# Kernel optimization log

Hardware: AMD Instinct MI355X
Metric: run time of the kernel (lower is better)

## Reference

```python
import jax, jax.numpy as jnp
import numpy as np
from jax import lax

H = W = 28

def _bilinear(img, yy, xx, zero_pad):
    # img [C,H,W]; yy/xx [H,W] fractional source coords
    y0 = jnp.floor(yy); x0 = jnp.floor(xx)
    wy = yy - y0; wx = xx - x0
    y0i = y0.astype(jnp.int32); x0i = x0.astype(jnp.int32)
    def gather(yi, xi):
        v = img[:, jnp.clip(yi, 0, H - 1), jnp.clip(xi, 0, W - 1)]
        if zero_pad:
            valid = ((yi >= 0) & (yi < H) & (xi >= 0) & (xi < W)).astype(img.dtype)
            v = v * valid[None]
        return v
    return (gather(y0i, x0i) * (1 - wy) * (1 - wx)
            + gather(y0i, x0i + 1) * (1 - wy) * wx
            + gather(y0i + 1, x0i) * wy * (1 - wx)
            + gather(y0i + 1, x0i + 1) * wy * wx)

def _crop_resize(img, crop, top, left):
    # bilinear resize of img[:, top:top+crop, left:left+crop] back to 28x28
    # (same math as F.interpolate align_corners=False with edge clamping)
    j = jnp.arange(H, dtype=jnp.float32) + 0.5
    src = jnp.clip(j * crop / H - 0.5, 0.0, crop - 1.0)
    yy, xx = jnp.meshgrid(src + top, src + left, indexing='ij')
    return _bilinear(img, yy, xx, zero_pad=False)

def _rotate(img, rad):
    # F.affine_grid/grid_sample, align_corners=False, zero padding
    c = (2.0 * jnp.arange(H, dtype=jnp.float32) + 1.0) / H - 1.0
    Yn, Xn = jnp.meshgrid(c, c, indexing='ij')
    cs, sn = jnp.cos(rad), jnp.sin(rad)
    xs = cs * Xn - sn * Yn
    ys = sn * Xn + cs * Yn
    ix = ((xs + 1.0) * W - 1.0) / 2.0
    iy = ((ys + 1.0) * H - 1.0) / 2.0
    return _bilinear(img, iy, ix, zero_pad=True)

def augment(x, key):
    # fully batched version of the per-sample python-loop augmentation
    B = x.shape[0]
    ks = jax.random.split(key, 11)
    u = lambda k: jax.random.uniform(k, (B,))
    crop = jnp.floor(28.0 * (0.7 + 0.3 * u(ks[0])))          # int(28*(0.7+0.3*r))
    top = jnp.floor((28.0 - crop) * u(ks[1]))
    left = jnp.floor((28.0 - crop) * u(ks[2]))
    x = jax.vmap(_crop_resize)(x, crop, top, left)
    flip = (u(ks[3]) < 0.5)[:, None, None, None]
    x = jnp.where(flip, x[..., ::-1], x)
    rot = (u(ks[4]) < 0.8)[:, None, None, None]
    rad = (20.0 * u(ks[5]) - 10.0) * jnp.pi / 180.0
    x = jnp.where(rot, jax.vmap(_rotate)(x, rad), x)
    cj = (u(ks[6]) < 0.8)[:, None, None, None]
    b = (0.2 * u(ks[7]) - 0.1)[:, None, None, None]
    c = (0.8 + 0.4 * u(ks[8]))[:, None, None, None]
    xj = jnp.clip((jnp.clip(x + b, 0.0, 1.0) - 0.5) * c + 0.5, 0.0, 1.0)
    x = jnp.where(cj, xj, x)
    na = (u(ks[9]) < 0.5)[:, None, None, None]
    noise = 0.05 * jax.random.normal(ks[10], x.shape, dtype=x.dtype)
    x = jnp.where(na, jnp.clip(x + noise, 0.0, 1.0), x)
    return (x - 0.5) / 0.5

def _conv(x, Wc, bc):
    y = lax.conv_general_dilated(x, Wc, (1, 1), 'SAME',
                                 dimension_numbers=('NCHW', 'OIHW', 'NCHW'))
    return y + bc[None, :, None, None]

def _maxpool2(x):
    return lax.reduce_window(x, -jnp.inf, lax.max, (1, 1, 2, 2), (1, 1, 2, 2), 'VALID')

def encoder(x, W1, b1, W2, b2, Wf, bf):
    h = _maxpool2(jax.nn.relu(_conv(x, W1, b1)))   # [B,32,14,14]
    h = _maxpool2(jax.nn.relu(_conv(h, W2, b2)))   # [B,64,7,7]
    h = h.reshape(h.shape[0], -1)                  # [B,3136]
    return h @ Wf.T + bf                           # [B,512]

def projector(h, Wp1, bp1, Wp2, bp2):
    return jax.nn.relu(h @ Wp1.T + bp1) @ Wp2.T + bp2

def setup_inputs() -> dict:
    key = jax.random.key(0)
    ks = jax.random.split(key, 12)
    B, FD, PD = 4096, 512, 128
    x = jax.random.uniform(ks[0], (B, 1, 28, 28), dtype=jnp.float32)
    s = lambda k, shp, fan: (jax.random.normal(k, shp, dtype=jnp.float32) * (1.0 / np.sqrt(fan)))
    return {
        'x': x,
        'W1': s(ks[1], (32, 1, 3, 3), 9), 'b1': jnp.zeros((32,), jnp.float32),
        'W2': s(ks[2], (64, 32, 3, 3), 32 * 9), 'b2': jnp.zeros((64,), jnp.float32),
        'Wf': s(ks[3], (FD, 64 * 7 * 7), 64 * 7 * 7), 'bf': jnp.zeros((FD,), jnp.float32),
        'Wp1': s(ks[4], (FD, FD), FD), 'bp1': jnp.zeros((FD,), jnp.float32),
        'Wp2': s(ks[5], (PD, FD), FD), 'bp2': jnp.zeros((PD,), jnp.float32),
    }

def reference(x, W1, b1, W2, b2, Wf, bf, Wp1, bp1, Wp2, bp2):
    akey = jax.random.key(42)
    k1, k2 = jax.random.split(akey)
    x1 = augment(x, k1)
    x2 = augment(x, k2)
    h1 = encoder(x1, W1, b1, W2, b2, Wf, bf)
    h2 = encoder(x2, W1, b1, W2, b2, Wf, bf)
    z1 = projector(h1, Wp1, bp1, Wp2, bp2)
    z2 = projector(h2, Wp1, bp1, Wp2, bp2)
    return (z1, z2)
```

## Files before the change

### kernel.cpp

```cpp
#include <hip/hip_runtime.h>
#include <stdint.h>
#include <math.h>

typedef __attribute__((ext_vector_type(8))) short bf16x8;
typedef __attribute__((ext_vector_type(4))) float f32x4;

__device__ __forceinline__ ushort f2bf(float f) {
    uint32_t u = __float_as_uint(f);
    u += 0x7fffu + ((u >> 16) & 1u);
    return (ushort)(u >> 16);
}

__device__ __forceinline__ uint32_t rotl32(uint32_t v, int r) {
    return (v << r) | (v >> (32 - r));
}

__device__ __forceinline__ void threefry(uint32_t k0, uint32_t k1,
                                         uint32_t c0, uint32_t c1,
                                         uint32_t& o0, uint32_t& o1) {
    uint32_t ks2 = k0 ^ k1 ^ 0x1BD11BDAu;
    uint32_t x0 = c0 + k0, x1 = c1 + k1;
    x0 += x1; x1 = rotl32(x1, 13); x1 ^= x0;
    x0 += x1; x1 = rotl32(x1, 15); x1 ^= x0;
    x0 += x1; x1 = rotl32(x1, 26); x1 ^= x0;
    x0 += x1; x1 = rotl32(x1,  6); x1 ^= x0;
    x0 += k1;  x1 += ks2 + 1u;
    x0 += x1; x1 = rotl32(x1, 17); x1 ^= x0;
    x0 += x1; x1 = rotl32(x1, 29); x1 ^= x0;
    x0 += x1; x1 = rotl32(x1, 16); x1 ^= x0;
    x0 += x1; x1 = rotl32(x1, 24); x1 ^= x0;
    x0 += ks2; x1 += k0 + 2u;
    x0 += x1; x1 = rotl32(x1, 13); x1 ^= x0;
    x0 += x1; x1 = rotl32(x1, 15); x1 ^= x0;
    x0 += x1; x1 = rotl32(x1, 26); x1 ^= x0;
    x0 += x1; x1 = rotl32(x1,  6); x1 ^= x0;
    x0 += k0;  x1 += k1 + 3u;
    x0 += x1; x1 = rotl32(x1, 17); x1 ^= x0;
    x0 += x1; x1 = rotl32(x1, 29); x1 ^= x0;
    x0 += x1; x1 = rotl32(x1, 16); x1 ^= x0;
    x0 += x1; x1 = rotl32(x1, 24); x1 ^= x0;
    x0 += k1;  x1 += ks2 + 4u;
    x0 += x1; x1 = rotl32(x1, 13); x1 ^= x0;
    x0 += x1; x1 = rotl32(x1, 15); x1 ^= x0;
    x0 += x1; x1 = rotl32(x1, 26); x1 ^= x0;
    x0 += x1; x1 = rotl32(x1,  6); x1 ^= x0;
    x0 += ks2; x1 += k0 + 5u;
    o0 = x0; o1 = x1;
}

__device__ __forceinline__ uint32_t rbits32(uint32_t k0, uint32_t k1, uint32_t idx) {
    uint32_t o0, o1;
    threefry(k0, k1, 0u, idx, o0, o1);
    return o0 ^ o1;
}

__device__ __forceinline__ float u01_from_bits(uint32_t bits) {
    return __uint_as_float((bits >> 9) | 0x3f800000u) - 1.0f;
}

__device__ float erfinv_xla(float x) {
    #pragma clang fp contract(off)
    float w = -log1pf(-x * x);
    float p;
    if (w < 5.0f) {
        w = w - 2.5f;
        p = 2.81022636e-08f;
        p = 3.43273939e-07f + p * w;
        p = -3.5233877e-06f + p * w;
        p = -4.39150654e-06f + p * w;
        p = 0.00021858087f + p * w;
        p = -0.00125372503f + p * w;
        p = -0.00417768164f + p * w;
        p = 0.246640727f + p * w;
        p = 1.50140941f + p * w;
    } else {
        w = sqrtf(w) - 3.0f;
        p = -0.000200214257f;
        p = 0.000100950558f + p * w;
        p = 0.00134934322f + p * w;
        p = -0.00367342844f + p * w;
        p = 0.00573950773f + p * w;
        p = -0.0076224613f + p * w;
        p = 0.00943887047f + p * w;
        p = 1.00167406f + p * w;
        p = 2.83297682f + p * w;
    }
    return p * x;
}

#define P_OFF      0
#define NK_OFF     98304
#define W2GT_OFF   98320
#define WFB_OFF    107792
#define WP1B_OFF   910608
#define WP2B_OFF   1041680
#define AUG_OFF    1074448
#define PL2_OFF    4285712
#define H_OFF      10708240

__global__ void param_kernel(float* __restrict__ P, uint32_t* __restrict__ NK) {
    #pragma clang fp contract(off)
    int gid = blockIdx.x * blockDim.x + threadIdx.x;
    if (gid >= 8192) return;
    int v = gid >> 12;
    int i = gid & 4095;

    uint32_t kv0, kv1;
    threefry(0u, 42u, 0u, (uint32_t)v, kv0, kv1);

    uint32_t sk0[11], sk1[11];
    #pragma unroll
    for (int j = 0; j < 11; ++j) threefry(kv0, kv1, 0u, (uint32_t)j, sk0[j], sk1[j]);

    float u[10];
    #pragma unroll
    for (int j = 0; j < 10; ++j) u[j] = u01_from_bits(rbits32(sk0[j], sk1[j], (uint32_t)i));

    float crop = floorf(28.0f * (0.7f + 0.3f * u[0]));
    float top  = floorf((28.0f - crop) * u[1]);
    float left = floorf((28.0f - crop) * u[2]);
    float flip = (u[3] < 0.5f) ? 1.0f : 0.0f;
    float rot  = (u[4] < 0.8f) ? 1.0f : 0.0f;
    float rad  = ((20.0f * u[5] - 10.0f) * 3.14159274101257324f) / 180.0f;
    float cj   = (u[6] < 0.8f) ? 1.0f : 0.0f;
    float bb   = 0.2f * u[7] - 0.1f;
    float cc   = 0.8f + 0.4f * u[8];
    float na   = (u[9] < 0.5f) ? 1.0f : 0.0f;

    float* p = P + gid * 12;
    p[0] = crop; p[1] = top; p[2] = left; p[3] = flip; p[4] = rot;
    p[5] = rad;  p[6] = cj;  p[7] = bb;   p[8] = cc;   p[9] = na;
    p[10] = cosf(rad); p[11] = sinf(rad);

    if (i == 0) { NK[v * 2] = sk0[10]; NK[v * 2 + 1] = sk1[10]; }
}

__global__ void wprep_w2(const float* __restrict__ W2, ushort* __restrict__ W2gT) {
    int idx = blockIdx.x * 256 + threadIdx.x;
    if (idx >= 64 * 296) return;
    int oc = idx / 296, k = idx % 296;
    float v = 0.0f;
    if (k < 288) {
        int s = k >> 5, ic = k & 31;
        int ky = s / 3, kx = s % 3;
        v = W2[((oc * 32 + ic) * 3 + ky) * 3 + kx];
    }
    W2gT[idx] = f2bf(v);
}

__global__ void wprep_wf(const float* __restrict__ Wf, ushort* __restrict__ WfB) {
    int idx = blockIdx.x * 256 + threadIdx.x;
    if (idx >= 512 * 3136) return;
    int n = idx / 3136, kp = idx % 3136;
    int pos = kp >> 6, oc = kp & 63;
    WfB[idx] = f2bf(Wf[n * 3136 + oc * 49 + pos]);
}

__global__ void wprep_cast(const float* __restrict__ src, ushort* __restrict__ dst, int n) {
    int idx = blockIdx.x * 256 + threadIdx.x;
    if (idx < n) dst[idx] = f2bf(src[idx]);
}

__global__ __launch_bounds__(256) void augment_kernel(const float* __restrict__ x,
                                                      const float* __restrict__ P,
                                                      const uint32_t* __restrict__ NK,
                                                      float* __restrict__ AUG, int v) {
    #pragma clang fp contract(off)
    int i = blockIdx.x;
    int r = v * 4096 + i;
    int t = threadIdx.x;
    __shared__ float img[784];
    __shared__ float s1[784];
    __shared__ float srctab[28];

    const float* p = P + r * 12;
    float crop = p[0], top = p[1], left = p[2];
    int flip = (p[3] != 0.0f);
    int rot  = (p[4] != 0.0f);
    int cj = (p[6] != 0.0f);
    float bb = p[7], cc = p[8];
    int na = (p[9] != 0.0f);
    float cs = p[10], sn = p[11];
    uint32_t nk0 = NK[v * 2], nk1 = NK[v * 2 + 1];

    for (int q = t; q < 784; q += 256) img[q] = x[i * 784 + q];
    if (t < 28) {
        float j = (float)t + 0.5f;
        float s = j * crop / 28.0f - 0.5f;
        srctab[t] = fminf(fmaxf(s, 0.0f), crop - 1.0f);
    }
    __syncthreads();

    for (int q = t; q < 784; q += 256) {
        int py = q / 28, px = q - (q / 28) * 28;
        int sxcol = flip ? (27 - px) : px;
        float yy = srctab[py] + top;
        float xx = srctab[sxcol] + left;
        float y0f = floorf(yy), x0f = floorf(xx);
        float wy = yy - y0f, wx = xx - x0f;
        int y0 = (int)y0f, x0 = (int)x0f;

        int yc0 = min(max(y0, 0), 27),     xc0 = min(max(x0, 0), 27);
        int yc1 = min(max(y0 + 1, 0), 27), xc1 = min(max(x0 + 1, 0), 27);
        float g00 = img[yc0 * 28 + xc0];
        float g01 = img[yc0 * 28 + xc1];
        float g10 = img[yc1 * 28 + xc0];
        float g11 = img[yc1 * 28 + xc1];
        float val = g00 * (1.0f - wy) * (1.0f - wx) + g01 * (1.0f - wy) * wx
                  + g10 * wy * (1.0f - wx) + g11 * wy * wx;
        s1[q] = val;
    }
    __syncthreads();

    for (int q = t; q < 784; q += 256) {
        int py = q / 28, px = q - (q / 28) * 28;
        float val;
        if (rot) {
            float Yn = (2.0f * (float)py + 1.0f) / 28.0f - 1.0f;
            float Xn = (2.0f * (float)px + 1.0f) / 28.0f - 1.0f;
            float xs = cs * Xn - sn * Yn;
            float ys = sn * Xn + cs * Yn;
            float ix = ((xs + 1.0f) * 28.0f - 1.0f) / 2.0f;
            float iy = ((ys + 1.0f) * 28.0f - 1.0f) / 2.0f;
            float y0f = floorf(iy), x0f = floorf(ix);
            float wy = iy - y0f, wx = ix - x0f;
            int y0 = (int)y0f, x0 = (int)x0f;
            float g[2][2];
            #pragma unroll
            for (int dy = 0; dy < 2; ++dy) {
                #pragma unroll
                for (int dx = 0; dx < 2; ++dx) {
                    int yi = y0 + dy, xi = x0 + dx;
                    int yc = min(max(yi, 0), 27), xc = min(max(xi, 0), 27);
                    float vv = s1[yc * 28 + xc];
                    float valid = (yi >= 0 && yi < 28 && xi >= 0 && xi < 28) ? 1.0f : 0.0f;
                    g[dy][dx] = vv * valid;
                }
            }
            val = g[0][0] * (1.0f - wy) * (1.0f - wx) + g[0][1] * (1.0f - wy) * wx
                + g[1][0] * wy * (1.0f - wx) + g[1][1] * wy * wx;
        } else {
            val = s1[q];
        }

        if (cj) {
            float vc = fminf(fmaxf(val + bb, 0.0f), 1.0f);
            val = fminf(fmaxf((vc - 0.5f) * cc + 0.5f, 0.0f), 1.0f);
        }

        if (na) {
            int idx = i * 784 + q;
            uint32_t bits = rbits32(nk0, nk1, (uint32_t)idx);
            float f = u01_from_bits(bits);
            const float lo = -0.99999994f;
            float uu = f * 2.0f + lo;
            uu = fmaxf(lo, uu);
            float n = 1.4142135623730951f * erfinv_xla(uu);
            val = fminf(fmaxf(val + 0.05f * n, 0.0f), 1.0f);
        }

        AUG[i * 784 + q] = (val - 0.5f) / 0.5f;
    }
}

__global__ __launch_bounds__(256) void conv12_kernel(
        const float* __restrict__ AUG,
        const float* __restrict__ W1, const float* __restrict__ b1,
        const ushort* __restrict__ W2gT, const float* __restrict__ b2,
        ushort* __restrict__ PL2) {
    int i = blockIdx.x, t = threadIdx.x;
    __shared__ __align__(16) ushort buf[12576];
    __shared__ __align__(16) ushort w1sT[32 * 32];
    ushort* A1   = buf;
    ushort* pl1p = buf;

    {
        int q0 = t * 4;
        #pragma unroll
        for (int j = 0; j < 4; ++j) {
            int q = q0 + j;
            int oc = q >> 5, k = q & 31;
            w1sT[q] = (k < 9) ? f2bf(W1[oc * 9 + k]) : (ushort)0;
        }
    }

    const float* Ai = AUG + (size_t)i * 784;
    if (t < 196) {
        int py = t / 14, px = t - (t / 14) * 14;
        int ybase = 2 * py - 1, xbase = 2 * px - 1;
        uint32_t u[4][4];
        #pragma unroll
        for (int ry = 0; ry < 4; ++ry) {
            int yy = ybase + ry;
            bool yok = (unsigned)yy < 28u;
            const float* rowp = Ai + yy * 28;
            #pragma unroll
            for (int rx = 0; rx < 4; ++rx) {
                int xx = xbase + rx;
                float vv = (yok && (unsigned)xx < 28u) ? rowp[xx] : 0.0f;
                u[ry][rx] = (uint32_t)f2bf(vv);
            }
        }
        #pragma unroll
        for (int w = 0; w < 4; ++w) {
            int dy = w >> 1, dx = w & 1;
            uint4 W0, W1v;
            W0.x = u[dy][dx]     | (u[dy][dx + 1] << 16);
            W0.y = u[dy][dx + 2] | (u[dy + 1][dx] << 16);
            W0.z = u[dy + 1][dx + 1] | (u[dy + 1][dx + 2] << 16);
            W0.w = u[dy + 2][dx]     | (u[dy + 2][dx + 1] << 16);
            W1v.x = u[dy + 2][dx + 2];
            W1v.y = 0; W1v.z = 0; W1v.w = 0;
            ((uint4*)A1)[(t * 4 + w) * 2]     = W0;
            ((uint4*)A1)[(t * 4 + w) * 2 + 1] = W1v;
        }
    }
    __syncthreads();

    int l = t & 63, wv = t >> 6;
    int lr = l & 15, lg = l >> 4;

    float m0r[13], m1r[13];
    {
        bf16x8 bA = *(const bf16x8*)(w1sT + lr * 32 + lg * 8);
        bf16x8 bB = *(const bf16x8*)(w1sT + (16 + lr) * 32 + lg * 8);
        #pragma unroll
        for (int it = 0; it < 13; ++it) {
            int tt = wv + it * 4;
            if (tt < 49) {
                bf16x8 af = *(const bf16x8*)(A1 + (tt * 16 + lr) * 16 + lg * 8);
                f32x4 a0 = {0.0f, 0.0f, 0.0f, 0.0f};
                f32x4 a1acc = {0.0f, 0.0f, 0.0f, 0.0f};
                a0    = __builtin_amdgcn_mfma_f32_16x16x32_bf16(af, bA, a0, 0, 0, 0);
                a1acc = __builtin_amdgcn_mfma_f32_16x16x32_bf16(af, bB, a1acc, 0, 0, 0);
                m0r[it] = fmaxf(fmaxf(a0[0], a0[1]), fmaxf(a0[2], a0[3]));
                m1r[it] = fmaxf(fmaxf(a1acc[0], a1acc[1]), fmaxf(a1acc[2], a1acc[3]));
            }
        }
    }
    __syncthreads();

    for (int q = t; q < 1440; q += 256) ((uint4*)pl1p)[q] = uint4{0, 0, 0, 0};
    __syncthreads();

    {
        float bia0 = b1[lr], bia1 = b1[16 + lr];
        #pragma unroll
        for (int it = 0; it < 13; ++it) {
            int tt = wv + it * 4;
            if (tt < 49) {
                int pidx = tt * 4 + lg;
                int py = pidx / 14, px = pidx - py * 14;
                int base = ((py + 1) * 18 + (px + 1)) * 40;
                pl1p[base + lr]      = f2bf(fmaxf(m0r[it] + bia0, 0.0f));
                pl1p[base + 16 + lr] = f2bf(fmaxf(m1r[it] + bia1, 0.0f));
            }
        }
    }
    __syncthreads();

    {
        bf16x8 bfr[9];
        #pragma unroll
        for (int s = 0; s < 9; ++s)
            bfr[s] = *(const bf16x8*)(W2gT + (wv * 16 + lr) * 296 + s * 32 + lg * 8);
        float bias2 = b2[wv * 16 + lr];

        #pragma unroll
        for (int pyp = 0; pyp < 7; ++pyp) {
            int py0 = pyp * 2;
            bf16x8 f[4][3];
            #pragma unroll
            for (int j = 0; j < 4; ++j)
                #pragma unroll
                for (int kx = 0; kx < 3; ++kx)
                    f[j][kx] = *(const bf16x8*)(pl1p + ((py0 + j) * 18 + (lr + kx)) * 40 + lg * 8);
            f32x4 acc0 = {bias2, bias2, bias2, bias2};
            f32x4 acc1 = acc0;
            #pragma unroll
            for (int ky = 0; ky < 3; ++ky)
                #pragma unroll
                for (int kx = 0; kx < 3; ++kx) {
                    acc0 = __builtin_amdgcn_mfma_f32_16x16x32_bf16(f[ky][kx],     bfr[ky * 3 + kx], acc0, 0, 0, 0);
                    acc1 = __builtin_amdgcn_mfma_f32_16x16x32_bf16(f[ky + 1][kx], bfr[ky * 3 + kx], acc1, 0, 0, 0);
                }
            float v0 = fmaxf(fmaxf(fmaxf(acc0[0], acc0[1]), fmaxf(acc1[0], acc1[1])), 0.0f);
            float v1 = fmaxf(fmaxf(fmaxf(acc0[2], acc0[3]), fmaxf(acc1[2], acc1[3])), 0.0f);
            int px0 = lg * 2, px1 = px0 + 1;
            size_t base = (size_t)i * 3136 + (size_t)(pyp * 7) * 64 + wv * 16 + lr;
            PL2[base + (size_t)px0 * 64] = f2bf(v0);
            if (px1 < 7) PL2[base + (size_t)px1 * 64] = f2bf(v1);
        }
    }
}

template<bool RELU, bool OUT_BF16>
__global__ __launch_bounds__(256) void gemm_bt_kernel(
        const ushort* __restrict__ A, const ushort* __restrict__ BT,
        const float* __restrict__ bias, void* __restrict__ Cout,
        int M, int N, int K) {
    __shared__ __align__(16) ushort lds[2][2][4096];
    int t = threadIdx.x;
    int w = t >> 6, l = t & 63;
    int lr = l & 15, lc = l >> 4;
    int wm = w >> 1, wn = w & 1;
    int bm = blockIdx.x, bn = blockIdx.y;
    int NKt = K >> 6;

    const ushort* Ab = A + (size_t)bm * 64 * K;
    const ushort* Bb = BT + (size_t)bn * 64 * K;

    int r0 = t >> 3, s0 = t & 7;
    int c1i = t + 256;
    int r1 = c1i >> 3, s1 = c1i & 7;
    int d0 = r0 * 8 + (s0 ^ (r0 & 7));
    int d1 = r1 * 8 + (s1 ^ (r1 & 7));

    f32x4 acc[2][2] = {};

    uint4 tA0, tA1, tB0, tB1;
    #define GLOAD(kt) do { \
        tA0 = *(const uint4*)(Ab + (size_t)r0 * K + (kt) * 64 + s0 * 8); \
        tA1 = *(const uint4*)(Ab + (size_t)r1 * K + (kt) * 64 + s1 * 8); \
        tB0 = *(const uint4*)(Bb + (size_t)r0 * K + (kt) * 64 + s0 * 8); \
        tB1 = *(const uint4*)(Bb + (size_t)r1 * K + (kt) * 64 + s1 * 8); } while (0)
    #define LWRITE(bufi) do { \
        ((uint4*)lds[bufi][0])[d0] = tA0; ((uint4*)lds[bufi][0])[d1] = tA1; \
        ((uint4*)lds[bufi][1])[d0] = tB0; ((uint4*)lds[bufi][1])[d1] = tB1; } while (0)

    GLOAD(0); LWRITE(0);
    int buf = 0;
    for (int kt = 0; kt < NKt; ++kt) {
        __syncthreads();
        if (kt + 1 < NKt) GLOAD(kt + 1);
        const ushort* Al = lds[buf][0];
        const ushort* Bl = lds[buf][1];
        #pragma unroll
        for (int ks = 0; ks < 2; ++ks) {
            bf16x8 af[2], bg[2];
            #pragma unroll
            for (int mt = 0; mt < 2; ++mt) {
                int row = wm * 32 + mt * 16 + lr;
                int unit = row * 8 + ((ks * 4 + lc) ^ (row & 7));
                af[mt] = *(const bf16x8*)(Al + unit * 8);
            }
            #pragma unroll
            for (int nt = 0; nt < 2; ++nt) {
                int row = wn * 32 + nt * 16 + lr;
                int unit = row * 8 + ((ks * 4 + lc) ^ (row & 7));
                bg[nt] = *(const bf16x8*)(Bl + unit * 8);
            }
            #pragma unroll
            for (int mt = 0; mt < 2; ++mt)
                #pragma unroll
                for (int nt = 0; nt < 2; ++nt)
                    acc[mt][nt] = __builtin_amdgcn_mfma_f32_16x16x32_bf16(af[mt], bg[nt], acc[mt][nt], 0, 0, 0);
        }
        if (kt + 1 < NKt) LWRITE(buf ^ 1);
        buf ^= 1;
    }

    #pragma unroll
    for (int nt = 0; nt < 2; ++nt) {
        int gcol = bn * 64 + wn * 32 + nt * 16 + lr;
        float bv = bias[gcol];
        #pragma unroll
        for (int mt = 0; mt < 2; ++mt) {
            #pragma unroll
            for (int rg = 0; rg < 4; ++rg) {
                int grow = bm * 64 + wm * 32 + mt * 16 + lc * 4 + rg;
                float vv = acc[mt][nt][rg] + bv;
                if (RELU) vv = fmaxf(vv, 0.0f);
                if (OUT_BF16) ((ushort*)Cout)[(size_t)grow * N + gcol] = f2bf(vv);
                else          ((float*)Cout)[(size_t)grow * N + gcol] = vv;
            }
        }
    }
    #undef GLOAD
    #undef LWRITE
}

extern "C" void kernel_launch(void* const* d_in, const int* in_sizes, int n_in,
                              void* d_out, int out_size, void* d_ws, size_t ws_size,
                              hipStream_t stream) {
    const float* x   = (const float*)d_in[0];
    const float* W1  = (const float*)d_in[1];
    const float* b1  = (const float*)d_in[2];
    const float* W2  = (const float*)d_in[3];
    const float* b2  = (const float*)d_in[4];
    const float* Wf  = (const float*)d_in[5];
    const float* bf  = (const float*)d_in[6];
    const float* Wp1 = (const float*)d_in[7];
    const float* bp1 = (const float*)d_in[8];
    const float* Wp2 = (const float*)d_in[9];
    const float* bp2 = (const float*)d_in[10];

    float* ws     = (float*)d_ws;
    float* P      = ws + P_OFF;
    uint32_t* NK  = (uint32_t*)(ws + NK_OFF);
    ushort* W2gT  = (ushort*)(ws + W2GT_OFF);
    ushort* WfB   = (ushort*)(ws + WFB_OFF);
    ushort* Wp1B  = (ushort*)(ws + WP1B_OFF);
    ushort* Wp2B  = (ushort*)(ws + WP2B_OFF);
    float* AUG    = ws + AUG_OFF;
    ushort* PL2   = (ushort*)(ws + PL2_OFF);
    ushort* Hb    = (ushort*)(ws + H_OFF);
    ushort* P1    = (ushort*)(ws + AUG_OFF);
    float* out    = (float*)d_out;

    param_kernel<<<32, 256, 0, stream>>>(P, NK);
    wprep_w2<<<74, 256, 0, stream>>>(W2, W2gT);
    wprep_wf<<<6272, 256, 0, stream>>>(Wf, WfB);
    wprep_cast<<<1024, 256, 0, stream>>>(Wp1, Wp1B, 512 * 512);
    wprep_cast<<<256, 256, 0, stream>>>(Wp2, Wp2B, 128 * 512);

    for (int v = 0; v < 2; ++v) {
        augment_kernel<<<4096, 256, 0, stream>>>(x, P, NK, AUG, v);
        conv12_kernel<<<4096, 256, 0, stream>>>(AUG, W1, b1, W2gT, b2, PL2);
        gemm_bt_kernel<false, true><<<dim3(64, 8), 256, 0, stream>>>(
            PL2, WfB, bf, Hb, 4096, 512, 3136);
        gemm_bt_kernel<true, true><<<dim3(64, 8), 256, 0, stream>>>(
            Hb, Wp1B, bp1, P1, 4096, 512, 512);
        gemm_bt_kernel<false, false><<<dim3(64, 2), 256, 0, stream>>>(
            P1, Wp2B, bp2, out + (size_t)v * 4096 * 128, 4096, 128, 512);
    }
}
```

Before: 261.4 us.

## Add 128x64-tile bf16 GEMM kernel for encoder FC and projector layer

Adds a new GEMM kernel with 128-row M tiles, where each wave computes a 64x32 output block (4x2 MFMA tiles). It uses swizzled LDS and register-staged double buffering, and is applied to the encoder FC and the first projector GEMM. The larger tile raises arithmetic intensity and halves the number of B-tile reloads across M. In exchange, the grid shrinks to 256 blocks, which may underfill the GPU's CUs, and register pressure goes up.

```diff
diff --git a/kernel.cpp b/kernel.cpp
--- a/kernel.cpp
+++ b/kernel.cpp
@@ -395,6 +395,97 @@
 }
 
 template<bool RELU, bool OUT_BF16>
+__global__ __launch_bounds__(256) void gemm_bt128_kernel(
+        const ushort* __restrict__ A, const ushort* __restrict__ BT,
+        const float* __restrict__ bias, void* __restrict__ Cout,
+        int M, int N, int K) {
+    __shared__ __align__(16) ushort lds[2][12288];
+    int t = threadIdx.x;
+    int w = t >> 6, l = t & 63;
+    int lr = l & 15, lc = l >> 4;
+    int wm = w >> 1, wn = w & 1;
+    int bm = blockIdx.x, bn = blockIdx.y;
+    int NKt = K >> 6;
+
+    const ushort* Ab = A + (size_t)bm * 128 * K;
+    const ushort* Bb = BT + (size_t)bn * 64 * K;
+
+    int rA[4], sA[4], dA[4];
+    #pragma unroll
+    for (int j = 0; j < 4; ++j) {
+        int idx = t + 256 * j;
+        rA[j] = idx >> 3; sA[j] = idx & 7;
+        dA[j] = rA[j] * 8 + (sA[j] ^ (rA[j] & 7));
+    }
+
+    f32x4 acc[4][2] = {};
+
+    uint4 tA[4], tB[2];
+    #define GLOAD(kt) do { \
+        tA[0] = *(const uint4*)(Ab + (size_t)rA[0] * K + (kt) * 64 + sA[0] * 8); \
+        tA[1] = *(const uint4*)(Ab + (size_t)rA[1] * K + (kt) * 64 + sA[1] * 8); \
+        tA[2] = *(const uint4*)(Ab + (size_t)rA[2] * K + (kt) * 64 + sA[2] * 8); \
+        tA[3] = *(const uint4*)(Ab + (size_t)rA[3] * K + (kt) * 64 + sA[3] * 8); \
+        tB[0] = *(const uint4*)(Bb + (size_t)rA[0] * K + (kt) * 64 + sA[0] * 8); \
+        tB[1] = *(const uint4*)(Bb + (size_t)rA[1] * K + (kt) * 64 + sA[1] * 8); } while (0)
+    #define LWRITE(bufi) do { \
+        ((uint4*)lds[bufi])[dA[0]] = tA[0]; ((uint4*)lds[bufi])[dA[1]] = tA[1]; \
+        ((uint4*)lds[bufi])[dA[2]] = tA[2]; ((uint4*)lds[bufi])[dA[3]] = tA[3]; \
+        ((uint4*)lds[bufi])[1024 + dA[0]] = tB[0]; ((uint4*)lds[bufi])[1024 + dA[1]] = tB[1]; } while (0)
+
+    GLOAD(0); LWRITE(0);
+    int buf = 0;
+    for (int kt = 0; kt < NKt; ++kt) {
+        __syncthreads();
+        if (kt + 1 < NKt) GLOAD(kt + 1);
+        const ushort* Al = lds[buf];
+        const ushort* Bl = lds[buf] + 8192;
+        #pragma unroll
+        for (int ks = 0; ks < 2; ++ks) {
+            bf16x8 af[4], bg[2];
+            #pragma unroll
+            for (int mt = 0; mt < 4; ++mt) {
+                int row = wm * 64 + mt * 16 + lr;
+                int unit = row * 8 + ((ks * 4 + lc) ^ (row & 7));
+                af[mt] = *(const bf16x8*)(Al + unit * 8);
+            }
+            #pragma unroll
+            for (int nt = 0; nt < 2; ++nt) {
+                int row = wn * 32 + nt * 16 + lr;
+                int unit = row * 8 + ((ks * 4 + lc) ^ (row & 7));
+                bg[nt] = *(const bf16x8*)(Bl + unit * 8);
+            }
+            #pragma unroll
+            for (int mt = 0; mt < 4; ++mt)
+                #pragma unroll
+                for (int nt = 0; nt < 2; ++nt)
+                    acc[mt][nt] = __builtin_amdgcn_mfma_f32_16x16x32_bf16(af[mt], bg[nt], acc[mt][nt], 0, 0, 0);
+        }
+        if (kt + 1 < NKt) LWRITE(buf ^ 1);
+        buf ^= 1;
+    }
+
+    #pragma unroll
+    for (int nt = 0; nt < 2; ++nt) {
+        int gcol = bn * 64 + wn * 32 + nt * 16 + lr;
+        float bv = bias[gcol];
+        #pragma unroll
+        for (int mt = 0; mt < 4; ++mt) {
+            #pragma unroll
+            for (int rg = 0; rg < 4; ++rg) {
+                int grow = bm * 128 + wm * 64 + mt * 16 + lc * 4 + rg;
+                float vv = acc[mt][nt][rg] + bv;
+                if (RELU) vv = fmaxf(vv, 0.0f);
+                if (OUT_BF16) ((ushort*)Cout)[(size_t)grow * N + gcol] = f2bf(vv);
+                else          ((float*)Cout)[(size_t)grow * N + gcol] = vv;
+            }
+        }
+    }
+    #undef GLOAD
+    #undef LWRITE
+}
+
+template<bool RELU, bool OUT_BF16>
 __global__ __launch_bounds__(256) void gemm_bt_kernel(
         const ushort* __restrict__ A, const ushort* __restrict__ BT,
         const float* __restrict__ bias, void* __restrict__ Cout,
@@ -517,9 +608,9 @@
     for (int v = 0; v < 2; ++v) {
         augment_kernel<<<4096, 256, 0, stream>>>(x, P, NK, AUG, v);
         conv12_kernel<<<4096, 256, 0, stream>>>(AUG, W1, b1, W2gT, b2, PL2);
-        gemm_bt_kernel<false, true><<<dim3(64, 8), 256, 0, stream>>>(
+        gemm_bt128_kernel<false, true><<<dim3(32, 8), 256, 0, stream>>>(
             PL2, WfB, bf, Hb, 4096, 512, 3136);
-        gemm_bt_kernel<true, true><<<dim3(64, 8), 256, 0, stream>>>(
+        gemm_bt128_kernel<true, true><<<dim3(32, 8), 256, 0, stream>>>(
             Hb, Wp1B, bp1, P1, 4096, 512, 512);
         gemm_bt_kernel<false, false><<<dim3(64, 2), 256, 0, stream>>>(
             P1, Wp2B, bp2, out + (size_t)v * 4096 * 128, 4096, 128, 512);
```

Result: slower. 410.5 us (+57.0%).
